# Optimization experiments

Measured on AMD Instinct MI355X. Metric: run time of the kernel, lower is better.

## Reference

```python
import jax, jax.numpy as jnp
import numpy as np

B, T, C, H, MEM = 2, 2048, 1024, 16, 256
HD = C // H


def setup_inputs() -> dict:
    key = jax.random.key(0)
    ks = jax.random.split(key, 6)
    return {
        "x": jax.random.normal(ks[0], (B, T, C), dtype=jnp.float32),
        "ext_mem": jax.random.normal(ks[1], (B, MEM, C), dtype=jnp.float32),
        "W_attn": jax.random.normal(ks[2], (C, 3 * C), dtype=jnp.float32) * 0.02,
        "b_attn": jax.random.normal(ks[3], (3 * C,), dtype=jnp.float32) * 0.02,
        "W_proj": jax.random.normal(ks[4], (C, C), dtype=jnp.float32) * 0.02,
        "b_proj": jax.random.normal(ks[5], (C,), dtype=jnp.float32) * 0.02,
    }


def reference(x, ext_mem, W_attn, b_attn, W_proj, b_proj):
    Bx, Tx, Cx = x.shape
    qkv = x @ W_attn + b_attn                      # [B,T,3C]
    q, k, v = jnp.split(qkv, 3, axis=-1)
    # [B,H,T,HD]
    q = q.reshape(Bx, Tx, H, HD).transpose(0, 2, 1, 3)
    k = k.reshape(Bx, Tx, H, HD).transpose(0, 2, 1, 3)
    v = v.reshape(Bx, Tx, H, HD).transpose(0, 2, 1, 3)
    mem = ext_mem.reshape(Bx, -1, H, HD).transpose(0, 2, 1, 3)  # [B,H,MEM,HD]
    k = jnp.concatenate([mem, k], axis=2)          # [B,H,MEM+T,HD]
    v = jnp.concatenate([mem, v], axis=2)
    mem_len = k.shape[2] - Tx
    scale = 1.0 / jnp.sqrt(jnp.float32(HD))
    att = jnp.einsum("bhtd,bhsd->bhts", q, k) * scale  # [B,H,T,MEM+T]
    # memory prefix fully attended; causal over the T query positions
    rows = jnp.arange(Tx)[:, None]
    cols = jnp.arange(mem_len + Tx)[None, :]
    allowed = (cols < mem_len) | ((cols - mem_len) <= rows)  # [T,MEM+T]
    att = jnp.where(allowed[None, None], att, jnp.float32(-jnp.inf))
    att = jax.nn.softmax(att, axis=-1)
    y = jnp.einsum("bhts,bhsd->bhtd", att, v)      # [B,H,T,HD]
    y = y.transpose(0, 2, 1, 3).reshape(Bx, Tx, Cx)
    return y @ W_proj + b_proj
```

## Files before the change

kernel.cpp:

```cpp
#include <hip/hip_runtime.h>

#define B_    2
#define T_    2048
#define C_    1024
#define H_    16
#define HD_   64
#define MEM_  256
#define S_    2304
#define NKT_  36

typedef __attribute__((ext_vector_type(8))) short short8;
typedef __attribute__((ext_vector_type(4))) short short4v;
typedef __attribute__((ext_vector_type(4))) float f32x4;

__device__ __forceinline__ unsigned short f2bf(float x) {
    return (unsigned short)((__float_as_uint(x) + 0x8000u) >> 16);
}

__device__ __forceinline__ unsigned int pk2bf(float lo, float hi) {
    unsigned int a = __float_as_uint(lo) + 0x8000u;
    unsigned int b = __float_as_uint(hi) + 0x8000u;
    return __builtin_amdgcn_perm(b, a, 0x07060302);
}

typedef const __attribute__((address_space(1))) unsigned int* gp_t;
typedef __attribute__((address_space(3))) unsigned int* lp_t;

__device__ __forceinline__ void gll16(const unsigned short* g, unsigned short* l) {
    __builtin_amdgcn_global_load_lds((gp_t)g, (lp_t)l, 16, 0, 0);
}

__global__ __launch_bounds__(256) void prep_all(
    const float* __restrict__ x, const float* __restrict__ Wa,
    const float* __restrict__ Wp, const float* __restrict__ ext,
    unsigned short* __restrict__ x_tl, unsigned short* __restrict__ WtA,
    unsigned short* __restrict__ WtP, unsigned short* __restrict__ k_ws,
    unsigned short* __restrict__ v_tl)
{
    __shared__ float L[64][65];
    const int bid = blockIdx.x, tid = threadIdx.x;
    if (bid < 4096) {
        int i = bid * 256 + tid;
        int c = (i & 255) * 4;
        int m = i >> 8;
        float4 v = ((const float4*)x)[i];
        ushort4 o;
        o.x = f2bf(v.x); o.y = f2bf(v.y); o.z = f2bf(v.z); o.w = f2bf(v.w);
        int mt = m >> 7, r = m & 127, kc = c >> 5, cc = c & 31;
        int p = (cc >> 3) ^ ((r >> 1) & 3);
        *(ushort4*)&x_tl[(((size_t)mt * 32 + kc) << 12) + (r << 5) + p * 8 + (cc & 7)] = o;
    } else if (bid < 5120) {
        const float* in; unsigned short* out; int Cc, r0, c0;
        if (bid < 4864) {
            int r = bid - 4096; in = Wa; out = WtA; Cc = 3 * C_;
            c0 = (r % 48) * 64; r0 = (r / 48) * 64;
        } else {
            int r = bid - 4864; in = Wp; out = WtP; Cc = C_;
            c0 = (r & 15) * 64; r0 = (r >> 4) * 64;
        }
        const int jj = tid >> 4;
        const int i4 = (tid & 15) * 4;
#pragma unroll
        for (int t = 0; t < 4; ++t) {
            int j = jj + t * 16;
            float4 v = *(const float4*)(in + (size_t)(r0 + j) * Cc + c0 + i4);
            L[i4 + 0][j] = v.x; L[i4 + 1][j] = v.y;
            L[i4 + 2][j] = v.z; L[i4 + 3][j] = v.w;
        }
        __syncthreads();
#pragma unroll
        for (int t = 0; t < 4; ++t) {
            int n = c0 + jj + t * 16;
            int k = r0 + i4;
            ushort4 o;
            o.x = f2bf(L[jj + t * 16][i4 + 0]); o.y = f2bf(L[jj + t * 16][i4 + 1]);
            o.z = f2bf(L[jj + t * 16][i4 + 2]); o.w = f2bf(L[jj + t * 16][i4 + 3]);
            int nt = n >> 7, r = n & 127, kc = k >> 5, cc = k & 31;
            int p = (cc >> 3) ^ ((r >> 1) & 3);
            *(ushort4*)&out[(((size_t)nt * 32 + kc) << 12) + (r << 5) + p * 8 + (cc & 7)] = o;
        }
    } else {
        int idx = (bid - 5120) * 256 + tid;
        float val = ext[idx];
        int c = idx & (C_ - 1), m = (idx >> 10) & (MEM_ - 1), b = idx >> 18;
        int h = c >> 6, d = c & 63;
        int bh = b * H_ + h;
        unsigned short bv = f2bf(val);
        k_ws[(size_t)bh * S_ * 64 + (size_t)m * 64 + (((d >> 3) ^ (m & 7)) << 3) + (d & 7)] = bv;
        int ts = m >> 6, key = m & 63;
        v_tl[(((size_t)bh * NKT_ + ts) * 64 + d) * 64 + (((key >> 3) ^ (d & 7)) << 3) + (key & 7)] = bv;
    }
}

template<int MODE>
__global__ __launch_bounds__(256) void gemm_mfma(
    const unsigned short* __restrict__ A,
    const unsigned short* __restrict__ Bt,
    const float* __restrict__ bias,
    unsigned short* __restrict__ q_ws,
    unsigned short* __restrict__ k_ws,
    unsigned short* __restrict__ v_tl,
    float* __restrict__ out)
{
    __shared__ __align__(16) unsigned short As[2][4096];
    __shared__ __align__(16) unsigned short Bs[2][4096];
    const int tid = threadIdx.x, lane = tid & 63, wave = tid >> 6;
    const int wr = wave >> 1, wc = wave & 1;
    const size_t abase = (size_t)blockIdx.y * 32 * 4096;
    const size_t bbase = (size_t)blockIdx.x * 32 * 4096;

    f32x4 acc[4][4];
#pragma unroll
    for (int i = 0; i < 4; ++i)
#pragma unroll
        for (int j = 0; j < 4; ++j) acc[i][j] = (f32x4){0.f, 0.f, 0.f, 0.f};

    auto stage = [&](int kc, int buf) {
        const unsigned short* ga = A + abase + (size_t)kc * 4096;
        const unsigned short* gb = Bt + bbase + (size_t)kc * 4096;
#pragma unroll
        for (int s = 0; s < 2; ++s) {
            int seg = wave + s * 4;
            gll16(ga + seg * 512 + lane * 8, &As[buf][seg * 512]);
            gll16(gb + seg * 512 + lane * 8, &Bs[buf][seg * 512]);
        }
    };

    stage(0, 0);
    __syncthreads();
    for (int kc = 0; kc < 32; ++kc) {
        if (kc + 1 < 32) stage(kc + 1, (kc + 1) & 1);
        const unsigned short* as = As[kc & 1];
        const unsigned short* bs = Bs[kc & 1];
        short8 af[4], bf4[4];
#pragma unroll
        for (int i = 0; i < 4; ++i) {
            int row = wr * 64 + i * 16 + (lane & 15);
            int ph = (lane >> 4) ^ ((row >> 1) & 3);
            af[i] = *(const short8*)&as[row * 32 + ph * 8];
        }
#pragma unroll
        for (int j = 0; j < 4; ++j) {
            int row = wc * 64 + j * 16 + (lane & 15);
            int ph = (lane >> 4) ^ ((row >> 1) & 3);
            bf4[j] = *(const short8*)&bs[row * 32 + ph * 8];
        }
#pragma unroll
        for (int i = 0; i < 4; ++i)
#pragma unroll
            for (int j = 0; j < 4; ++j)
                acc[i][j] = __builtin_amdgcn_mfma_f32_16x16x32_bf16(
                    af[i], bf4[j], acc[i][j], 0, 0, 0);
        __syncthreads();
    }

    if (MODE == 0) {
#pragma unroll
        for (int j = 0; j < 4; ++j) {
            int n = blockIdx.x * 128 + wc * 64 + j * 16 + (lane & 15);
            float bs = bias[n];
            int sel = n >> 10, h = (n >> 6) & 15, d = n & 63;
#pragma unroll
            for (int i = 0; i < 4; ++i) {
                int m = blockIdx.y * 128 + wr * 64 + i * 16 + (lane >> 4) * 4;
                int b = m >> 11, t0 = m & (T_ - 1);
                int bh = b * H_ + h;
                if (sel == 0) {
                    size_t base = ((size_t)bh * T_ + t0) * 64 + d;
#pragma unroll
                    for (int r = 0; r < 4; ++r)
                        q_ws[base + (size_t)r * 64] = f2bf(acc[i][j][r] + bs);
                } else if (sel == 1) {
#pragma unroll
                    for (int r = 0; r < 4; ++r) {
                        int s = MEM_ + t0 + r;
                        k_ws[(size_t)bh * S_ * 64 + (size_t)s * 64
                             + (((d >> 3) ^ (s & 7)) << 3) + (d & 7)] =
                            f2bf(acc[i][j][r] + bs);
                    }
                } else {
                    int s0 = MEM_ + t0, ts = s0 >> 6, key = s0 & 63;
                    ushort4 pv;
                    pv.x = f2bf(acc[i][j][0] + bs);
                    pv.y = f2bf(acc[i][j][1] + bs);
                    pv.z = f2bf(acc[i][j][2] + bs);
                    pv.w = f2bf(acc[i][j][3] + bs);
                    *(ushort4*)&v_tl[(((size_t)bh * NKT_ + ts) * 64 + d) * 64
                                     + (((key >> 3) ^ (d & 7)) << 3) + (key & 7)] = pv;
                }
            }
        }
    } else {
#pragma unroll
        for (int j = 0; j < 4; ++j) {
            int n = blockIdx.x * 128 + wc * 64 + j * 16 + (lane & 15);
            float bs = bias[n];
#pragma unroll
            for (int i = 0; i < 4; ++i) {
                int m = blockIdx.y * 128 + wr * 64 + i * 16 + (lane >> 4) * 4;
#pragma unroll
                for (int r = 0; r < 4; ++r)
                    out[(size_t)(m + r) * C_ + n] = acc[i][j][r] + bs;
            }
        }
    }
}

__global__ __launch_bounds__(256) void flash_mfma(
    const unsigned short* __restrict__ qg,
    const unsigned short* __restrict__ kg,
    const unsigned short* __restrict__ vg,
    unsigned short* __restrict__ yt)
{
    __shared__ __align__(16) unsigned short Ks[2][4096];
    __shared__ __align__(16) unsigned short Vs[2][4096];

    const int tid = threadIdx.x, lane = tid & 63, wave = tid >> 6;
    const int quad = lane >> 4;
    const int a = blockIdx.x;
    const int h = blockIdx.y, b = blockIdx.z;
    const int qtA = a, qtB = 31 - a;
    const int ntA = 5 + qtA, ntB = 5 + qtB;
    const int bh = b * H_ + h;
    const size_t kbase = (size_t)bh * S_ * 64;
    const size_t vbase = (size_t)bh * NKT_ * 4096;

    short8 qfA[2], qfB[2];
    {
        const unsigned short* p = qg + ((size_t)bh * T_ + qtA * 64 + wave * 16
                                        + (lane & 15)) * 64 + quad * 8;
        qfA[0] = *(const short8*)p; qfA[1] = *(const short8*)(p + 32);
        p = qg + ((size_t)bh * T_ + qtB * 64 + wave * 16
                  + (lane & 15)) * 64 + quad * 8;
        qfB[0] = *(const short8*)p; qfB[1] = *(const short8*)(p + 32);
    }

    f32x4 oA[4], oB[4];
#pragma unroll
    for (int j = 0; j < 4; ++j) {
        oA[j] = (f32x4){0.f, 0.f, 0.f, 0.f};
        oB[j] = (f32x4){0.f, 0.f, 0.f, 0.f};
    }
    float lA = 0.f, lB = 0.f;

    auto stage = [&](int kt, int buf) {
        const unsigned short* gk = kg + kbase + (size_t)kt * 4096;
        const unsigned short* gv = vg + vbase + (size_t)kt * 4096;
#pragma unroll
        for (int s = 0; s < 2; ++s) {
            int seg = wave + s * 4;
            gll16(gk + seg * 512 + lane * 8, &Ks[buf][seg * 512]);
            gll16(gv + seg * 512 + lane * 8, &Vs[buf][seg * 512]);
        }
    };

    const float C1 = 0.18033688011112042f;

    stage(0, 0);
    __syncthreads();
    for (int kt = 0; kt < ntB; ++kt) {
        const int buf = kt & 1;
        if (kt + 1 < ntB) stage(kt + 1, buf ^ 1);
        const unsigned short* ks = Ks[buf];
        const unsigned short* vs = Vs[buf];
        const int s0 = kt * 64;

        short8 kA[4][2];
#pragma unroll
        for (int kb = 0; kb < 4; ++kb)
#pragma unroll
            for (int ksub = 0; ksub < 2; ++ksub) {
                int key = kb * 16 + (lane & 15);
                int ph = (ksub * 4 + quad) ^ (lane & 7);
                kA[kb][ksub] = *(const short8*)&ks[key * 64 + ph * 8];
            }
        short4v vB[4][4];
#pragma unroll
        for (int kb = 0; kb < 4; ++kb)
#pragma unroll
            for (int dblk = 0; dblk < 4; ++dblk) {
                int d = dblk * 16 + (lane & 15);
                int ph = (kb * 2 + (lane >> 5)) ^ (d & 7);
                vB[kb][dblk] = *(const short4v*)&vs[d * 64 + ph * 8 + (quad & 1) * 4];
            }

        auto process = [&](const short8* qf, f32x4* o, float& l, int qt0, bool diag) {
#pragma unroll
            for (int kb = 0; kb < 4; ++kb) {
                f32x4 z = (f32x4){0.f, 0.f, 0.f, 0.f};
                z = __builtin_amdgcn_mfma_f32_16x16x32_bf16(kA[kb][0], qf[0], z, 0, 0, 0);
                z = __builtin_amdgcn_mfma_f32_16x16x32_bf16(kA[kb][1], qf[1], z, 0, 0, 0);
                float p[4];
#pragma unroll
                for (int r = 0; r < 4; ++r) {
                    float e = exp2f(z[r] * C1);
                    if (diag) {
                        int key = s0 + kb * 16 + quad * 4 + r;
                        int t = qt0 + wave * 16 + (lane & 15);
                        if (key - MEM_ > t) e = 0.f;
                    }
                    l += e;
                    p[r] = e;
                }
                unsigned int r01 = pk2bf(p[0], p[1]);
                unsigned int r23 = pk2bf(p[2], p[3]);
                short4v pf;
                *(unsigned int*)&pf = r01;
                *((unsigned int*)&pf + 1) = r23;
#pragma unroll
                for (int dblk = 0; dblk < 4; ++dblk)
                    o[dblk] = __builtin_amdgcn_mfma_f32_16x16x16bf16_1k(
                        pf, vB[kb][dblk], o[dblk], 0, 0, 0);
            }
        };

        if (kt < ntA) process(qfA, oA, lA, qtA * 64, kt == ntA - 1);
        process(qfB, oB, lB, qtB * 64, kt == ntB - 1);
        __syncthreads();
    }

    auto finish = [&](f32x4* o, float l, int qt0) {
        l += __shfl_xor(l, 16);
        l += __shfl_xor(l, 32);
        float linv[4];
#pragma unroll
        for (int r = 0; r < 4; ++r)
            linv[r] = 1.f / __shfl(l, quad * 4 + r);
#pragma unroll
        for (int dblk = 0; dblk < 4; ++dblk) {
            int c = h * 64 + dblk * 16 + (lane & 15);
            int kc = c >> 5, cc = c & 31;
#pragma unroll
            for (int r = 0; r < 4; ++r) {
                int t = qt0 + wave * 16 + quad * 4 + r;
                int m = b * T_ + t;
                int mt = m >> 7, rr = m & 127;
                int p = (cc >> 3) ^ ((rr >> 1) & 3);
                yt[(((size_t)mt * 32 + kc) << 12) + (rr << 5) + p * 8 + (cc & 7)] =
                    f2bf(o[dblk][r] * linv[r]);
            }
        }
    };
    finish(oA, lA, qtA * 64);
    finish(oB, lB, qtB * 64);
}

extern "C" void kernel_launch(void* const* d_in, const int* in_sizes, int n_in,
                              void* d_out, int out_size, void* d_ws, size_t ws_size,
                              hipStream_t stream) {
    (void)in_sizes; (void)n_in; (void)out_size; (void)ws_size;
    const float* x      = (const float*)d_in[0];
    const float* ext    = (const float*)d_in[1];
    const float* W_attn = (const float*)d_in[2];
    const float* b_attn = (const float*)d_in[3];
    const float* W_proj = (const float*)d_in[4];
    const float* b_proj = (const float*)d_in[5];
    float* out = (float*)d_out;

    unsigned short* x_tl  = (unsigned short*)d_ws;
    unsigned short* WtA   = x_tl + 4194304;
    unsigned short* WtP   = WtA + 3145728;
    unsigned short* q_ws  = WtP + 1048576;
    unsigned short* k_ws  = q_ws + 4194304;
    unsigned short* v_tl  = k_ws + 4718592;
    unsigned short* y_tl  = v_tl + 4718592;

    dim3 blk(256);
    prep_all<<<7168, blk, 0, stream>>>(x, W_attn, W_proj, ext,
                                       x_tl, WtA, WtP, k_ws, v_tl);
    gemm_mfma<0><<<dim3(24, 32), blk, 0, stream>>>(
        x_tl, WtA, b_attn, q_ws, k_ws, v_tl, nullptr);
    flash_mfma<<<dim3(16, H_, B_), blk, 0, stream>>>(q_ws, k_ws, v_tl, y_tl);
    gemm_mfma<1><<<dim3(8, 32), blk, 0, stream>>>(
        y_tl, WtP, b_proj, nullptr, nullptr, nullptr, out);
}
```

Before: 213.5 us.

## Split paired query tiles across two wave groups in 512-thread flash blocks

The flash attention kernel previously had each of 4 waves handle two query tiles (a and 31-a) serially per key tile. Now blocks have 8 waves: the first four handle tile a, the second four handle tile 31-a, sharing the same staged K/V tiles in LDS. This doubles wave-level parallelism and halves per-wave register state and serial MFMA work. In exchange, the short-tile waves sit idle but still join the barriers until the longer tile finishes, and each wave now loads its own K/V fragments, which doubles LDS read traffic.

After: 216.8 us. About the same (+1.5%).

```diff
diff --git a/kernel.cpp b/kernel.cpp
--- a/kernel.cpp
+++ b/kernel.cpp
@@ -206,7 +206,7 @@
     }
 }
 
-__global__ __launch_bounds__(256) void flash_mfma(
+__global__ __launch_bounds__(512) void flash_mfma(
     const unsigned short* __restrict__ qg,
     const unsigned short* __restrict__ kg,
     const unsigned short* __restrict__ vg,
@@ -216,75 +216,69 @@
     __shared__ __align__(16) unsigned short Vs[2][4096];
 
     const int tid = threadIdx.x, lane = tid & 63, wave = tid >> 6;
+    const int half = wave >> 2, wq = wave & 3;
     const int quad = lane >> 4;
     const int a = blockIdx.x;
     const int h = blockIdx.y, b = blockIdx.z;
-    const int qtA = a, qtB = 31 - a;
-    const int ntA = 5 + qtA, ntB = 5 + qtB;
+    const int qt = half ? (31 - a) : a;
+    const int nt = 5 + qt;
+    const int ntMax = 36 - a;
     const int bh = b * H_ + h;
     const size_t kbase = (size_t)bh * S_ * 64;
     const size_t vbase = (size_t)bh * NKT_ * 4096;
 
-    short8 qfA[2], qfB[2];
+    short8 qf[2];
     {
-        const unsigned short* p = qg + ((size_t)bh * T_ + qtA * 64 + wave * 16
+        const unsigned short* p = qg + ((size_t)bh * T_ + qt * 64 + wq * 16
                                         + (lane & 15)) * 64 + quad * 8;
-        qfA[0] = *(const short8*)p; qfA[1] = *(const short8*)(p + 32);
-        p = qg + ((size_t)bh * T_ + qtB * 64 + wave * 16
-                  + (lane & 15)) * 64 + quad * 8;
-        qfB[0] = *(const short8*)p; qfB[1] = *(const short8*)(p + 32);
-    }
-
-    f32x4 oA[4], oB[4];
-#pragma unroll
-    for (int j = 0; j < 4; ++j) {
-        oA[j] = (f32x4){0.f, 0.f, 0.f, 0.f};
-        oB[j] = (f32x4){0.f, 0.f, 0.f, 0.f};
-    }
-    float lA = 0.f, lB = 0.f;
+        qf[0] = *(const short8*)p; qf[1] = *(const short8*)(p + 32);
+    }
+
+    f32x4 o[4];
+#pragma unroll
+    for (int j = 0; j < 4; ++j) o[j] = (f32x4){0.f, 0.f, 0.f, 0.f};
+    float l = 0.f;
 
     auto stage = [&](int kt, int buf) {
         const unsigned short* gk = kg + kbase + (size_t)kt * 4096;
         const unsigned short* gv = vg + vbase + (size_t)kt * 4096;
-#pragma unroll
-        for (int s = 0; s < 2; ++s) {
-            int seg = wave + s * 4;
-            gll16(gk + seg * 512 + lane * 8, &Ks[buf][seg * 512]);
-            gll16(gv + seg * 512 + lane * 8, &Vs[buf][seg * 512]);
-        }
+        gll16(gk + wave * 512 + lane * 8, &Ks[buf][wave * 512]);
+        gll16(gv + wave * 512 + lane * 8, &Vs[buf][wave * 512]);
     };
 
     const float C1 = 0.18033688011112042f;
+    const int tq = qt * 64 + wq * 16 + (lane & 15);
 
     stage(0, 0);
     __syncthreads();
-    for (int kt = 0; kt < ntB; ++kt) {
+    for (int kt = 0; kt < ntMax; ++kt) {
         const int buf = kt & 1;
-        if (kt + 1 < ntB) stage(kt + 1, buf ^ 1);
-        const unsigned short* ks = Ks[buf];
-        const unsigned short* vs = Vs[buf];
-        const int s0 = kt * 64;
-
-        short8 kA[4][2];
-#pragma unroll
-        for (int kb = 0; kb < 4; ++kb)
-#pragma unroll
-            for (int ksub = 0; ksub < 2; ++ksub) {
-                int key = kb * 16 + (lane & 15);
-                int ph = (ksub * 4 + quad) ^ (lane & 7);
-                kA[kb][ksub] = *(const short8*)&ks[key * 64 + ph * 8];
-            }
-        short4v vB[4][4];
-#pragma unroll
-        for (int kb = 0; kb < 4; ++kb)
-#pragma unroll
-            for (int dblk = 0; dblk < 4; ++dblk) {
-                int d = dblk * 16 + (lane & 15);
-                int ph = (kb * 2 + (lane >> 5)) ^ (d & 7);
-                vB[kb][dblk] = *(const short4v*)&vs[d * 64 + ph * 8 + (quad & 1) * 4];
-            }
-
-        auto process = [&](const short8* qf, f32x4* o, float& l, int qt0, bool diag) {
+        if (kt + 1 < ntMax) stage(kt + 1, buf ^ 1);
+        if (kt < nt) {
+            const unsigned short* ks = Ks[buf];
+            const unsigned short* vs = Vs[buf];
+            const int s0 = kt * 64;
+            const bool diag = (kt == nt - 1);
+
+            short8 kA[4][2];
+#pragma unroll
+            for (int kb = 0; kb < 4; ++kb)
+#pragma unroll
+                for (int ksub = 0; ksub < 2; ++ksub) {
+                    int key = kb * 16 + (lane & 15);
+                    int ph = (ksub * 4 + quad) ^ (lane & 7);
+                    kA[kb][ksub] = *(const short8*)&ks[key * 64 + ph * 8];
+                }
+            short4v vB[4][4];
+#pragma unroll
+            for (int kb = 0; kb < 4; ++kb)
+#pragma unroll
+                for (int dblk = 0; dblk < 4; ++dblk) {
+                    int d = dblk * 16 + (lane & 15);
+                    int ph = (kb * 2 + (lane >> 5)) ^ (d & 7);
+                    vB[kb][dblk] = *(const short4v*)&vs[d * 64 + ph * 8 + (quad & 1) * 4];
+                }
+
 #pragma unroll
             for (int kb = 0; kb < 4; ++kb) {
                 f32x4 z = (f32x4){0.f, 0.f, 0.f, 0.f};
@@ -296,8 +290,7 @@
                     float e = exp2f(z[r] * C1);
                     if (diag) {
                         int key = s0 + kb * 16 + quad * 4 + r;
-                        int t = qt0 + wave * 16 + (lane & 15);
-                        if (key - MEM_ > t) e = 0.f;
+                        if (key - MEM_ > tq) e = 0.f;
                     }
                     l += e;
                     p[r] = e;
@@ -312,37 +305,30 @@
                     o[dblk] = __builtin_amdgcn_mfma_f32_16x16x16bf16_1k(
                         pf, vB[kb][dblk], o[dblk], 0, 0, 0);
             }
-        };
-
-        if (kt < ntA) process(qfA, oA, lA, qtA * 64, kt == ntA - 1);
-        process(qfB, oB, lB, qtB * 64, kt == ntB - 1);
+        }
         __syncthreads();
     }
 
-    auto finish = [&](f32x4* o, float l, int qt0) {
-        l += __shfl_xor(l, 16);
-        l += __shfl_xor(l, 32);
-        float linv[4];
-#pragma unroll
-        for (int r = 0; r < 4; ++r)
-            linv[r] = 1.f / __shfl(l, quad * 4 + r);
-#pragma unroll
-        for (int dblk = 0; dblk < 4; ++dblk) {
-            int c = h * 64 + dblk * 16 + (lane & 15);
-            int kc = c >> 5, cc = c & 31;
-#pragma unroll
-            for (int r = 0; r < 4; ++r) {
-                int t = qt0 + wave * 16 + quad * 4 + r;
-                int m = b * T_ + t;
-                int mt = m >> 7, rr = m & 127;
-                int p = (cc >> 3) ^ ((rr >> 1) & 3);
-                yt[(((size_t)mt * 32 + kc) << 12) + (rr << 5) + p * 8 + (cc & 7)] =
-                    f2bf(o[dblk][r] * linv[r]);
-            }
-        }
-    };
-    finish(oA, lA, qtA * 64);
-    finish(oB, lB, qtB * 64);
+    l += __shfl_xor(l, 16);
+    l += __shfl_xor(l, 32);
+    float linv[4];
+#pragma unroll
+    for (int r = 0; r < 4; ++r)
+        linv[r] = 1.f / __shfl(l, quad * 4 + r);
+#pragma unroll
+    for (int dblk = 0; dblk < 4; ++dblk) {
+        int c = h * 64 + dblk * 16 + (lane & 15);
+        int kc = c >> 5, cc = c & 31;
+#pragma unroll
+        for (int r = 0; r < 4; ++r) {
+            int t = qt * 64 + wq * 16 + quad * 4 + r;
+            int m = b * T_ + t;
+            int mt = m >> 7, rr = m & 127;
+            int p = (cc >> 3) ^ ((rr >> 1) & 3);
+            yt[(((size_t)mt * 32 + kc) << 12) + (rr << 5) + p * 8 + (cc & 7)] =
+                f2bf(o[dblk][r] * linv[r]);
+        }
+    }
 }
 
 extern "C" void kernel_launch(void* const* d_in, const int* in_sizes, int n_in,
@@ -370,7 +356,7 @@
                                        x_tl, WtA, WtP, k_ws, v_tl);
     gemm_mfma<0><<<dim3(24, 32), blk, 0, stream>>>(
         x_tl, WtA, b_attn, q_ws, k_ws, v_tl, nullptr);
-    flash_mfma<<<dim3(16, H_, B_), blk, 0, stream>>>(q_ws, k_ws, v_tl, y_tl);
+    flash_mfma<<<dim3(16, H_, B_), dim3(512), 0, stream>>>(q_ws, k_ws, v_tl, y_tl);
     gemm_mfma<1><<<dim3(8, 32), blk, 0, stream>>>(
         y_tl, WtP, b_proj, nullptr, nullptr, nullptr, out);
 }
```
